# Performance work log

Hardware: AMD Instinct MI355X
Metric: run time of the kernel (lower is better)

## Reference

```python
import jax, jax.numpy as jnp
import numpy as np

S, B, I, H, L = 512, 64, 512, 512, 2
EPS = 1e-5


def setup_inputs() -> dict:
    key = jax.random.key(0)
    ks = jax.random.split(key, 8)
    gain = float(np.sqrt(1.0 / H))
    u = lambda k, shp: jax.random.uniform(k, shp, jnp.float32, -gain, gain)
    return {
        "inputs": jax.random.normal(ks[0], (S, B, I), jnp.float32),
        "h0": jnp.zeros((L, B, H), jnp.float32),
        "c0": jnp.zeros((L, B, H), jnp.float32),
        "wx0": u(ks[1], (I, 4 * H)),
        "wx1": u(ks[2], (H, 4 * H)),
        "wh0": u(ks[3], (H, 4 * H)),
        "wh1": u(ks[4], (H, 4 * H)),
        "bias": u(ks[5], (L, 4 * H)),
        "ln_gamma": jnp.ones((L, 4, H), jnp.float32),
        "ln_beta": jnp.zeros((L, 4, H), jnp.float32),
    }


def _layer(x, h, c, wx, wh, b, gamma, beta):
    # Precompute the input projection as one big GEMM: [S,B,4H]
    xg = jnp.einsum('sbi,ig->sbg', x, wx) + b

    def cell(carry, xg_t):
        h, c = carry
        gate = xg_t + h @ wh                      # [B, 4H]
        g = gate.reshape(B, 4, H)
        mu = jnp.mean(g, axis=-1, keepdims=True)
        var = jnp.var(g, axis=-1, keepdims=True)
        g = (g - mu) * jax.lax.rsqrt(var + EPS) * gamma + beta
        i, f, o, u = g[:, 0], g[:, 1], g[:, 2], g[:, 3]
        c = jax.nn.sigmoid(f) * c + jax.nn.sigmoid(i) * jnp.tanh(u)
        h = jax.nn.sigmoid(o) * jnp.tanh(c)
        return (h, c), h

    (h, c), ys = jax.lax.scan(cell, (h, c), xg)
    return ys, h, c


def reference(inputs, h0, c0, wx0, wx1, wh0, wh1, bias, ln_gamma, ln_beta):
    x = inputs
    wxs, whs = [wx0, wx1], [wh0, wh1]
    hs, cs = [], []
    for l in range(L):
        x, h, c = _layer(x, h0[l], c0[l], wxs[l], whs[l], bias[l], ln_gamma[l], ln_beta[l])
        hs.append(h)
        cs.append(c)
    return x, jnp.stack(hs, 0), jnp.stack(cs, 0)
```

## Files before the change

### kernel.cpp

```cpp
#include <hip/hip_runtime.h>


#define NTH 256

typedef float f32x4 __attribute__((ext_vector_type(4)));

__device__ __forceinline__ float sigm(float x) { return 1.f / (1.f + __expf(-x)); }
__device__ __forceinline__ float tanh_f(float x) { return 2.f / (1.f + __expf(-2.f * x)) - 1.f; }

__device__ __forceinline__ unsigned long long pack2(float a, float b) {
  union { float f[2]; unsigned long long u; } x; x.f[0] = a; x.f[1] = b; return x.u;
}
__device__ __forceinline__ float lo2(unsigned long long u) {
  union { unsigned long long u; float f[2]; } x; x.u = u; return x.f[0];
}
__device__ __forceinline__ float hi2(unsigned long long u) {
  union { unsigned long long u; float f[2]; } x; x.u = u; return x.f[1];
}
__device__ __forceinline__ void sys_store64(unsigned long long* p, unsigned long long v) {
  __hip_atomic_store(p, v, __ATOMIC_RELAXED, __HIP_MEMORY_SCOPE_SYSTEM);
}
__device__ __forceinline__ unsigned long long sys_load64(const unsigned long long* p) {
  return __hip_atomic_load(p, __ATOMIC_RELAXED, __HIP_MEMORY_SCOPE_SYSTEM);
}

__device__ __forceinline__ void post(unsigned int* flag, unsigned int val) {
  __syncthreads();
  if (threadIdx.x == 0)
    __hip_atomic_store(flag, val, __ATOMIC_RELEASE, __HIP_MEMORY_SCOPE_SYSTEM);
}

__device__ __forceinline__ void waitall(const unsigned int* flags, unsigned int target) {
  long guard = 0;
  for (;;) {
    int ok = 1;
    if (threadIdx.x < 128) {
      unsigned int v = __hip_atomic_load(&flags[threadIdx.x * 32],
                                         __ATOMIC_RELAXED, __HIP_MEMORY_SCOPE_SYSTEM);
      ok = (v >= target);
    }
    if (__syncthreads_and(ok)) break;
    if (++guard > (1L << 22)) break;
  }
  __atomic_signal_fence(__ATOMIC_ACQUIRE);
}

__global__ __launch_bounds__(NTH, 1)
void lstm_pk(const float* __restrict__ inputs, const float* __restrict__ h0,
             const float* __restrict__ c0,
             const float* __restrict__ wx0, const float* __restrict__ wx1,
             const float* __restrict__ wh0, const float* __restrict__ wh1,
             const float* __restrict__ bias, const float* __restrict__ gamma_,
             const float* __restrict__ beta_,
             float* __restrict__ out,
             unsigned int* flags,
             unsigned long long* slots,
             float* __restrict__ h_state)
{
  extern __shared__ float lds[];
  float* W_lds = lds;
  float* A_lds = lds + 16384;
  float* part  = lds + 16384 + 17408;
  float* gates = part + 4352;
  float* minv  = gates + 1024;

  const int tid = threadIdx.x;
  const int wg = blockIdx.x;
  const int layer = wg >> 7;
  const int w = wg & 127;
  const int wavet = tid >> 6;
  const int lane = tid & 63;
  const int rq = lane & 15;
  const int gq = lane >> 4;
  const int srow = tid >> 2;
  const int sg = tid & 3;
  const int hc = 4 * w + sg;

  const float* Wx = layer ? wx1 : wx0;
  const float* Wh = layer ? wh1 : wh0;

  for (int i = 0; i < 16; ++i) {
    int e = tid + i * 256;
    int k = e >> 2, g = e & 3;
    const float* src = (k < 512) ? (Wx + (size_t)k * 2048)
                                 : (Wh + (size_t)(k - 512) * 2048);
    f32x4 v = *(const f32x4*)(src + g * 512 + 4 * w);
    *(f32x4*)&W_lds[k * 16 + g * 4] = v;
  }

  f32x4 biasr = *(const f32x4*)(bias + layer * 2048 + sg * 512 + 4 * w);
  float gam[4], bet[4];
#pragma unroll
  for (int g = 0; g < 4; ++g) {
    gam[g] = gamma_[layer * 2048 + g * 512 + hc];
    bet[g] = beta_[layer * 2048 + g * 512 + hc];
  }
  float c_st = c0[layer * 32768 + srow * 512 + hc];

  unsigned long long* slotL = slots + (size_t)layer * 32768;
  float* hstL = h_state + layer * 32768;
  unsigned int* fmyL = flags + layer * 4096;
  unsigned int* myflag = fmyL + w * 32;
  const unsigned int* fL0 = flags;

  const int strow = rq + 16 * wavet;
  const int first = layer ? 4 : 0;

  for (int t = 0; t < 512; ++t) {
    const unsigned int t2 = 2u * (unsigned)t;
    const float* xsrc = (layer ? out : inputs) + (size_t)t * 32768;
    const float* hsrc = (t == 0) ? (h0 + layer * 32768) : hstL;

    if (layer == 1 && t > 0) waitall(fmyL, t2);

    f32x4 acc[4];
#pragma unroll
    for (int r = 0; r < 4; ++r) acc[r] = (f32x4){0.f, 0.f, 0.f, 0.f};

    f32x4 st[8];
    auto LOADC = [&](int c) {
      const int koff = (c & 3) * 128;
      if (c < 4 && layer == 0) {
        const float* src = xsrc + strow * 512 + koff;
#pragma unroll
        for (int i = 0; i < 8; ++i) {
          int kq = gq + 4 * i;
          st[i] = *(const f32x4*)(src + 4 * kq);
        }
      } else {
        const float* src = ((c >= 4) ? hsrc : xsrc) + strow * 512 + koff;
        const unsigned long long* s64 = (const unsigned long long*)src;
#pragma unroll
        for (int i = 0; i < 8; ++i) {
          int kq = gq + 4 * i;
          unsigned long long a = sys_load64(&s64[2 * kq]);
          unsigned long long b = sys_load64(&s64[2 * kq + 1]);
          st[i][0] = lo2(a); st[i][1] = hi2(a);
          st[i][2] = lo2(b); st[i][3] = hi2(b);
        }
      }
    };
    auto WRITEC = [&](int b) {
      float* dst = A_lds + b * 8704;
#pragma unroll
      for (int i = 0; i < 8; ++i) {
        int kq = gq + 4 * i;
#pragma unroll
        for (int j = 0; j < 4; ++j)
          dst[(4 * kq + j) * 68 + strow] = st[i][j];
      }
    };
    auto COMPUTEC = [&](int c, int b) {
      const float* Ab = A_lds + b * 8704;
      const int kg = c * 128 + wavet * 32;
#pragma unroll 8
      for (int kk = 0; kk < 32; ++kk) {
        int k = wavet * 32 + kk;
        f32x4 av = *(const f32x4*)&Ab[k * 68 + 4 * rq];
        f32x4 wv = *(const f32x4*)&W_lds[(kg + kk) * 16 + gq * 4];
        acc[0] += av[0] * wv;
        acc[1] += av[1] * wv;
        acc[2] += av[2] * wv;
        acc[3] += av[3] * wv;
      }
    };

    LOADC(first);
    WRITEC(0);
    __syncthreads();
#pragma unroll 1
    for (int co = 0; co < 8; ++co) {
      int c = (co + first) & 7;
      if (co < 7) {
        if (co == 3) {
          if (layer == 1) waitall(fL0, t2 + 2u);
          else if (t > 0) waitall(fmyL, t2);
        }
        LOADC((c + 1) & 7);
      }
      COMPUTEC(c, co & 1);
      if (co < 7) WRITEC((co + 1) & 1);
      __syncthreads();
    }

#pragma unroll
    for (int r = 0; r < 4; ++r)
#pragma unroll
      for (int cc = 0; cc < 4; ++cc)
        part[(wavet * 64 + 4 * rq + r) * 17 + gq * 4 + cc] = acc[r][cc];
    __syncthreads();

    {
      f32x4 pre;
#pragma unroll
      for (int cc = 0; cc < 4; ++cc) {
        float v = biasr[cc];
        v += part[(0 * 64 + srow) * 17 + sg * 4 + cc];
        v += part[(1 * 64 + srow) * 17 + sg * 4 + cc];
        v += part[(2 * 64 + srow) * 17 + sg * 4 + cc];
        v += part[(3 * 64 + srow) * 17 + sg * 4 + cc];
        pre[cc] = v;
      }
      *(f32x4*)&gates[srow * 16 + sg * 4] = pre;
      float s = ((pre[0] + pre[1]) + pre[2]) + pre[3];
      float ss = ((pre[0] * pre[0] + pre[1] * pre[1]) + pre[2] * pre[2]) + pre[3] * pre[3];
      sys_store64(&slotL[(size_t)w * 256 + tid], pack2(s, ss));
    }
    post(myflag, t2 + 1u);
    waitall(fmyL, t2 + 1u);

    {
      float Sc[8], SSc[8];
#pragma unroll
      for (int j = 0; j < 8; ++j) { Sc[j] = 0.f; SSc[j] = 0.f; }
#pragma unroll 4
      for (int q8 = 0; q8 < 16; ++q8) {
#pragma unroll
        for (int j = 0; j < 8; ++j) {
          unsigned long long u = sys_load64(&slotL[(size_t)(q8 * 8 + j) * 256 + tid]);
          Sc[j] += lo2(u); SSc[j] += hi2(u);
        }
      }
      float S = ((Sc[0] + Sc[1]) + (Sc[2] + Sc[3])) + ((Sc[4] + Sc[5]) + (Sc[6] + Sc[7]));
      float SS = ((SSc[0] + SSc[1]) + (SSc[2] + SSc[3])) + ((SSc[4] + SSc[5]) + (SSc[6] + SSc[7]));
      float mu = S * (1.f / 512.f);
      float var = SS * (1.f / 512.f) - mu * mu;
      minv[tid * 2 + 0] = mu;
      minv[tid * 2 + 1] = rsqrtf(fmaxf(var, 0.f) + 1e-5f);
    }
    __syncthreads();

    {
      float gv[4];
#pragma unroll
      for (int g = 0; g < 4; ++g) {
        float pre = gates[srow * 16 + g * 4 + sg];
        gv[g] = (pre - minv[(srow * 4 + g) * 2]) * minv[(srow * 4 + g) * 2 + 1] * gam[g] + bet[g];
      }
      float ig = sigm(gv[0]);
      float fg = sigm(gv[1]);
      float og = sigm(gv[2]);
      float ug = tanh_f(gv[3]);
      c_st = fg * c_st + ig * ug;
      float hv = og * tanh_f(c_st);

      float hv2 = __shfl_down(hv, 1);
      float cv2 = __shfl_down(c_st, 1);
      if ((sg & 1) == 0) {
        unsigned long long hp = pack2(hv, hv2);
        sys_store64((unsigned long long*)&hstL[srow * 512 + hc], hp);
        sys_store64((unsigned long long*)&out[(size_t)t * 32768 + srow * 512 + hc], hp);
        if (t == 511) {
          sys_store64((unsigned long long*)&out[16777216 + layer * 32768 + srow * 512 + hc], hp);
          sys_store64((unsigned long long*)&out[16842752 + layer * 32768 + srow * 512 + hc],
                      pack2(c_st, cv2));
        }
      }
    }
    post(myflag, t2 + 2u);
  }
}

extern "C" void kernel_launch(void* const* d_in, const int* in_sizes, int n_in,
                              void* d_out, int out_size, void* d_ws, size_t ws_size,
                              hipStream_t stream) {
  const float* inputs = (const float*)d_in[0];
  const float* h0 = (const float*)d_in[1];
  const float* c0 = (const float*)d_in[2];
  const float* wx0 = (const float*)d_in[3];
  const float* wx1 = (const float*)d_in[4];
  const float* wh0 = (const float*)d_in[5];
  const float* wh1 = (const float*)d_in[6];
  const float* bias = (const float*)d_in[7];
  const float* gamma_ = (const float*)d_in[8];
  const float* beta_ = (const float*)d_in[9];
  float* out = (float*)d_out;

  char* ws = (char*)d_ws;
  unsigned int* flags = (unsigned int*)ws;
  unsigned long long* slots = (unsigned long long*)(ws + 65536);
  float* h_state = (float*)(ws + 65536 + 524288);

  const int smem_bytes = 158720;
  hipFuncSetAttribute((const void*)lstm_pk,
                      hipFuncAttributeMaxDynamicSharedMemorySize, smem_bytes);
  hipMemsetAsync(ws, 0, 65536, stream);

  hipLaunchKernelGGL(lstm_pk, dim3(256), dim3(NTH), smem_bytes, stream,
                     inputs, h0, c0, wx0, wx1, wh0, wh1, bias, gamma_, beta_,
                     out, flags, slots, h_state);
}
```

Measured before the change: 21.61 ms.

## Use fixed-point atomic LN stat reduction and retile per-step GEMM with smaller chunks

The layer-norm statistics are now reduced with 64-bit fixed-point atomicAdds into a double-buffered global accumulator. Previously each of 128 workgroups wrote its partial sums to slots and every workgroup then read all 128 of them. The per-timestep GEMM is retiled: 64-wide K chunks (16 per step), an 8x8 register tile per thread, a split-K partial reduction through LDS, and plain vector loads instead of system-scope atomic loads, with acquire fences added after the waits. This is meant to cut the cross-workgroup reduction traffic and the latency per timestep. In exchange it adds quantization error in the statistics and atomic contention on shared addresses. It also relies on zeroing the next step's buffer while other workgroups may still be using it.

```diff
diff --git a/kernel.cpp b/kernel.cpp
--- a/kernel.cpp
+++ b/kernel.cpp
@@ -8,20 +8,14 @@
 __device__ __forceinline__ float sigm(float x) { return 1.f / (1.f + __expf(-x)); }
 __device__ __forceinline__ float tanh_f(float x) { return 2.f / (1.f + __expf(-2.f * x)) - 1.f; }
 
+__device__ __forceinline__ void sys_store64(unsigned long long* p, unsigned long long v) {
+  __hip_atomic_store(p, v, __ATOMIC_RELAXED, __HIP_MEMORY_SCOPE_SYSTEM);
+}
+__device__ __forceinline__ unsigned long long sys_load64(const unsigned long long* p) {
+  return __hip_atomic_load(p, __ATOMIC_RELAXED, __HIP_MEMORY_SCOPE_SYSTEM);
+}
 __device__ __forceinline__ unsigned long long pack2(float a, float b) {
   union { float f[2]; unsigned long long u; } x; x.f[0] = a; x.f[1] = b; return x.u;
-}
-__device__ __forceinline__ float lo2(unsigned long long u) {
-  union { unsigned long long u; float f[2]; } x; x.u = u; return x.f[0];
-}
-__device__ __forceinline__ float hi2(unsigned long long u) {
-  union { unsigned long long u; float f[2]; } x; x.u = u; return x.f[1];
-}
-__device__ __forceinline__ void sys_store64(unsigned long long* p, unsigned long long v) {
-  __hip_atomic_store(p, v, __ATOMIC_RELAXED, __HIP_MEMORY_SCOPE_SYSTEM);
-}
-__device__ __forceinline__ unsigned long long sys_load64(const unsigned long long* p) {
-  return __hip_atomic_load(p, __ATOMIC_RELAXED, __HIP_MEMORY_SCOPE_SYSTEM);
 }
 
 __device__ __forceinline__ void post(unsigned int* flag, unsigned int val) {
@@ -54,24 +48,25 @@
              const float* __restrict__ beta_,
              float* __restrict__ out,
              unsigned int* flags,
-             unsigned long long* slots,
+             unsigned long long* stat_ws,
              float* __restrict__ h_state)
 {
   extern __shared__ float lds[];
   float* W_lds = lds;
   float* A_lds = lds + 16384;
-  float* part  = lds + 16384 + 17408;
-  float* gates = part + 4352;
+  float* part  = lds + 16384 + 8704;
+  float* gates = part + 8704;
   float* minv  = gates + 1024;
 
   const int tid = threadIdx.x;
   const int wg = blockIdx.x;
   const int layer = wg >> 7;
   const int w = wg & 127;
-  const int wavet = tid >> 6;
-  const int lane = tid & 63;
-  const int rq = lane & 15;
-  const int gq = lane >> 4;
+  const int cb = tid & 1;
+  const int ra = (tid >> 1) & 7;
+  const int m  = tid >> 4;
+  const int strow = tid & 63;
+  const int kq4 = tid >> 6;
   const int srow = tid >> 2;
   const int sg = tid & 3;
   const int hc = 4 * w + sg;
@@ -97,71 +92,68 @@
   }
   float c_st = c0[layer * 32768 + srow * 512 + hc];
 
-  unsigned long long* slotL = slots + (size_t)layer * 32768;
   float* hstL = h_state + layer * 32768;
   unsigned int* fmyL = flags + layer * 4096;
   unsigned int* myflag = fmyL + w * 32;
   const unsigned int* fL0 = flags;
 
-  const int strow = rq + 16 * wavet;
-  const int first = layer ? 4 : 0;
+  const int first = layer ? 8 : 0;
 
   for (int t = 0; t < 512; ++t) {
     const unsigned int t2 = 2u * (unsigned)t;
     const float* xsrc = (layer ? out : inputs) + (size_t)t * 32768;
     const float* hsrc = (t == 0) ? (h0 + layer * 32768) : hstL;
-
-    if (layer == 1 && t > 0) waitall(fmyL, t2);
-
-    f32x4 acc[4];
-#pragma unroll
-    for (int r = 0; r < 4; ++r) acc[r] = (f32x4){0.f, 0.f, 0.f, 0.f};
-
-    f32x4 st[8];
+    unsigned long long* statbuf = stat_ws + ((size_t)(t & 1) * 2 + layer) * 512;
+
+    if (layer == 1) {
+      waitall(fmyL, t2);
+      __builtin_amdgcn_fence(__ATOMIC_ACQUIRE, "agent");
+    }
+
+    f32x4 acc[8][2];
+#pragma unroll
+    for (int r = 0; r < 8; ++r) {
+      acc[r][0] = (f32x4){0.f, 0.f, 0.f, 0.f};
+      acc[r][1] = (f32x4){0.f, 0.f, 0.f, 0.f};
+    }
+
+    f32x4 st[4];
     auto LOADC = [&](int c) {
-      const int koff = (c & 3) * 128;
-      if (c < 4 && layer == 0) {
-        const float* src = xsrc + strow * 512 + koff;
-#pragma unroll
-        for (int i = 0; i < 8; ++i) {
-          int kq = gq + 4 * i;
-          st[i] = *(const f32x4*)(src + 4 * kq);
-        }
-      } else {
-        const float* src = ((c >= 4) ? hsrc : xsrc) + strow * 512 + koff;
-        const unsigned long long* s64 = (const unsigned long long*)src;
-#pragma unroll
-        for (int i = 0; i < 8; ++i) {
-          int kq = gq + 4 * i;
-          unsigned long long a = sys_load64(&s64[2 * kq]);
-          unsigned long long b = sys_load64(&s64[2 * kq + 1]);
-          st[i][0] = lo2(a); st[i][1] = hi2(a);
-          st[i][2] = lo2(b); st[i][3] = hi2(b);
-        }
-      }
+      const float* src = (c >= 8) ? (hsrc + strow * 512 + (c - 8) * 64)
+                                  : (xsrc + strow * 512 + c * 64);
+#pragma unroll
+      for (int i = 0; i < 4; ++i)
+        st[i] = *(const f32x4*)(src + 4 * (kq4 + 4 * i));
     };
     auto WRITEC = [&](int b) {
-      float* dst = A_lds + b * 8704;
-#pragma unroll
-      for (int i = 0; i < 8; ++i) {
-        int kq = gq + 4 * i;
+      float* dst = A_lds + b * 4352;
+#pragma unroll
+      for (int i = 0; i < 4; ++i) {
+        int kk = 4 * (kq4 + 4 * i);
 #pragma unroll
         for (int j = 0; j < 4; ++j)
-          dst[(4 * kq + j) * 68 + strow] = st[i][j];
+          dst[(kk + j) * 68 + strow] = st[i][j];
       }
     };
     auto COMPUTEC = [&](int c, int b) {
-      const float* Ab = A_lds + b * 8704;
-      const int kg = c * 128 + wavet * 32;
-#pragma unroll 8
-      for (int kk = 0; kk < 32; ++kk) {
-        int k = wavet * 32 + kk;
-        f32x4 av = *(const f32x4*)&Ab[k * 68 + 4 * rq];
-        f32x4 wv = *(const f32x4*)&W_lds[(kg + kk) * 16 + gq * 4];
-        acc[0] += av[0] * wv;
-        acc[1] += av[1] * wv;
-        acc[2] += av[2] * wv;
-        acc[3] += av[3] * wv;
+      const float* Ab = A_lds + b * 4352;
+      const int kW = (c < 8 ? c * 64 : 512 + (c - 8) * 64) + 4 * m;
+      const int kA = 4 * m;
+#pragma unroll
+      for (int kk = 0; kk < 4; ++kk) {
+        const float* arow = &Ab[(kA + kk) * 68 + 8 * ra];
+        f32x4 av0 = *(const f32x4*)arow;
+        f32x4 av1 = *(const f32x4*)(arow + 4);
+        const float* wrow = &W_lds[(kW + kk) * 16 + 8 * cb];
+        f32x4 wv0 = *(const f32x4*)wrow;
+        f32x4 wv1 = *(const f32x4*)(wrow + 4);
+#pragma unroll
+        for (int r = 0; r < 4; ++r) {
+          acc[r][0] += av0[r] * wv0;
+          acc[r][1] += av0[r] * wv1;
+          acc[r + 4][0] += av1[r] * wv0;
+          acc[r + 4][1] += av1[r] * wv1;
+        }
       }
     };
 
@@ -169,64 +161,77 @@
     WRITEC(0);
     __syncthreads();
 #pragma unroll 1
-    for (int co = 0; co < 8; ++co) {
-      int c = (co + first) & 7;
-      if (co < 7) {
-        if (co == 3) {
-          if (layer == 1) waitall(fL0, t2 + 2u);
-          else if (t > 0) waitall(fmyL, t2);
+    for (int co = 0; co < 16; ++co) {
+      int c = (co + first) & 15;
+      if (co < 15) {
+        if (co == 7) {
+          if (layer == 1) {
+            waitall(fL0, t2 + 2u);
+            __builtin_amdgcn_fence(__ATOMIC_ACQUIRE, "agent");
+          } else {
+            waitall(fmyL, t2);
+            __builtin_amdgcn_fence(__ATOMIC_ACQUIRE, "agent");
+          }
         }
-        LOADC((c + 1) & 7);
+        LOADC((c + 1) & 15);
       }
       COMPUTEC(c, co & 1);
-      if (co < 7) WRITEC((co + 1) & 1);
+      if (co < 15) WRITEC((co + 1) & 1);
       __syncthreads();
     }
 
-#pragma unroll
-    for (int r = 0; r < 4; ++r)
-#pragma unroll
-      for (int cc = 0; cc < 4; ++cc)
-        part[(wavet * 64 + 4 * rq + r) * 17 + gq * 4 + cc] = acc[r][cc];
-    __syncthreads();
-
-    {
-      f32x4 pre;
-#pragma unroll
-      for (int cc = 0; cc < 4; ++cc) {
-        float v = biasr[cc];
-        v += part[(0 * 64 + srow) * 17 + sg * 4 + cc];
-        v += part[(1 * 64 + srow) * 17 + sg * 4 + cc];
-        v += part[(2 * 64 + srow) * 17 + sg * 4 + cc];
-        v += part[(3 * 64 + srow) * 17 + sg * 4 + cc];
-        pre[cc] = v;
-      }
+    if (m >= 8) {
+      float* pg = part + (size_t)(m - 8) * 1088;
+#pragma unroll
+      for (int r = 0; r < 8; ++r) {
+        *(f32x4*)&pg[(8 * ra + r) * 17 + 8 * cb] = acc[r][0];
+        *(f32x4*)&pg[(8 * ra + r) * 17 + 8 * cb + 4] = acc[r][1];
+      }
+    }
+    __syncthreads();
+    if (m < 8) {
+      float* pg = part + (size_t)m * 1088;
+#pragma unroll
+      for (int r = 0; r < 8; ++r) {
+        float* p0 = &pg[(8 * ra + r) * 17 + 8 * cb];
+        f32x4 v0 = *(f32x4*)p0 + acc[r][0];
+        f32x4 v1 = *(f32x4*)(p0 + 4) + acc[r][1];
+        *(f32x4*)p0 = v0;
+        *(f32x4*)(p0 + 4) = v1;
+      }
+    }
+    __syncthreads();
+
+    {
+      f32x4 pre = biasr;
+#pragma unroll
+      for (int g = 0; g < 8; ++g)
+        pre += *(const f32x4*)&part[(size_t)g * 1088 + srow * 17 + sg * 4];
       *(f32x4*)&gates[srow * 16 + sg * 4] = pre;
       float s = ((pre[0] + pre[1]) + pre[2]) + pre[3];
       float ss = ((pre[0] * pre[0] + pre[1] * pre[1]) + pre[2] * pre[2]) + pre[3] * pre[3];
-      sys_store64(&slotL[(size_t)w * 256 + tid], pack2(s, ss));
+      atomicAdd(&statbuf[2 * tid],
+                (unsigned long long)(long long)llrintf(s * 1048576.f));
+      atomicAdd(&statbuf[2 * tid + 1],
+                (unsigned long long)(long long)llrintf(ss * 1048576.f));
     }
     post(myflag, t2 + 1u);
     waitall(fmyL, t2 + 1u);
 
     {
-      float Sc[8], SSc[8];
-#pragma unroll
-      for (int j = 0; j < 8; ++j) { Sc[j] = 0.f; SSc[j] = 0.f; }
-#pragma unroll 4
-      for (int q8 = 0; q8 < 16; ++q8) {
-#pragma unroll
-        for (int j = 0; j < 8; ++j) {
-          unsigned long long u = sys_load64(&slotL[(size_t)(q8 * 8 + j) * 256 + tid]);
-          Sc[j] += lo2(u); SSc[j] += hi2(u);
-        }
-      }
-      float S = ((Sc[0] + Sc[1]) + (Sc[2] + Sc[3])) + ((Sc[4] + Sc[5]) + (Sc[6] + Sc[7]));
-      float SS = ((SSc[0] + SSc[1]) + (SSc[2] + SSc[3])) + ((SSc[4] + SSc[5]) + (SSc[6] + SSc[7]));
-      float mu = S * (1.f / 512.f);
-      float var = SS * (1.f / 512.f) - mu * mu;
-      minv[tid * 2 + 0] = mu;
-      minv[tid * 2 + 1] = rsqrtf(fmaxf(var, 0.f) + 1e-5f);
+      unsigned long long* zb = stat_ws + ((size_t)((t + 1) & 1) * 2 + layer) * 512;
+      if (tid < 4) sys_store64(&zb[4 * w + tid], 0ull);
+    }
+
+    {
+      long long S = (long long)sys_load64(&statbuf[2 * tid]);
+      long long SS = (long long)sys_load64(&statbuf[2 * tid + 1]);
+      float Sf = (float)S * (1.f / 1048576.f);
+      float SSf = (float)SS * (1.f / 1048576.f);
+      float mu = Sf * (1.f / 512.f);
+      float var = SSf * (1.f / 512.f) - mu * mu;
+      minv[2 * tid + 0] = mu;
+      minv[2 * tid + 1] = rsqrtf(fmaxf(var, 0.f) + 1e-5f);
     }
     __syncthreads();
 
@@ -278,15 +283,15 @@
 
   char* ws = (char*)d_ws;
   unsigned int* flags = (unsigned int*)ws;
-  unsigned long long* slots = (unsigned long long*)(ws + 65536);
-  float* h_state = (float*)(ws + 65536 + 524288);
-
-  const int smem_bytes = 158720;
+  unsigned long long* stat_ws = (unsigned long long*)(ws + 65536);
+  float* h_state = (float*)(ws + 65536 + 16384);
+
+  const int smem_bytes = 141312;
   hipFuncSetAttribute((const void*)lstm_pk,
                       hipFuncAttributeMaxDynamicSharedMemorySize, smem_bytes);
-  hipMemsetAsync(ws, 0, 65536, stream);
+  hipMemsetAsync(ws, 0, 65536 + 16384, stream);
 
   hipLaunchKernelGGL(lstm_pk, dim3(256), dim3(NTH), smem_bytes, stream,
                      inputs, h0, c0, wx0, wx1, wh0, wh1, bias, gamma_, beta_,
-                     out, flags, slots, h_state);
-}
+                     out, flags, stat_ws, h_state);
+}
```

After: 21.67 ms. Within noise of the previous version (+0.3%).

## Overlap next-step input projection with LayerNorm stat exchange; use plain loads after fences

Applied to the files above, without the earlier changes.

Splits each step's gate GEMM into an input part (x·Wx) and a recurrent part (h·Wh). The x·Wx part for step t+1 is computed while waiting for the cross-block LayerNorm statistics barrier of step t, which takes it off the serial recurrent path. System-scope atomic 64-bit loads are replaced by ordinary vector loads preceded by agent-scope acquire fences. This relies on the fences being enough for cross-block visibility, and it keeps an extra accumulator set live in registers.

```diff
diff --git a/kernel.cpp b/kernel.cpp
--- a/kernel.cpp
+++ b/kernel.cpp
@@ -11,17 +11,8 @@
 __device__ __forceinline__ unsigned long long pack2(float a, float b) {
   union { float f[2]; unsigned long long u; } x; x.f[0] = a; x.f[1] = b; return x.u;
 }
-__device__ __forceinline__ float lo2(unsigned long long u) {
-  union { unsigned long long u; float f[2]; } x; x.u = u; return x.f[0];
-}
-__device__ __forceinline__ float hi2(unsigned long long u) {
-  union { unsigned long long u; float f[2]; } x; x.u = u; return x.f[1];
-}
 __device__ __forceinline__ void sys_store64(unsigned long long* p, unsigned long long v) {
   __hip_atomic_store(p, v, __ATOMIC_RELAXED, __HIP_MEMORY_SCOPE_SYSTEM);
-}
-__device__ __forceinline__ unsigned long long sys_load64(const unsigned long long* p) {
-  return __hip_atomic_load(p, __ATOMIC_RELAXED, __HIP_MEMORY_SCOPE_SYSTEM);
 }
 
 __device__ __forceinline__ void post(unsigned int* flag, unsigned int val) {
@@ -104,90 +95,80 @@
   const unsigned int* fL0 = flags;
 
   const int strow = rq + 16 * wavet;
-  const int first = layer ? 4 : 0;
-
-  for (int t = 0; t < 512; ++t) {
-    const unsigned int t2 = 2u * (unsigned)t;
-    const float* xsrc = (layer ? out : inputs) + (size_t)t * 32768;
-    const float* hsrc = (t == 0) ? (h0 + layer * 32768) : hstL;
-
-    if (layer == 1 && t > 0) waitall(fmyL, t2);
-
-    f32x4 acc[4];
-#pragma unroll
-    for (int r = 0; r < 4; ++r) acc[r] = (f32x4){0.f, 0.f, 0.f, 0.f};
-
-    f32x4 st[8];
-    auto LOADC = [&](int c) {
-      const int koff = (c & 3) * 128;
-      if (c < 4 && layer == 0) {
-        const float* src = xsrc + strow * 512 + koff;
-#pragma unroll
-        for (int i = 0; i < 8; ++i) {
-          int kq = gq + 4 * i;
-          st[i] = *(const f32x4*)(src + 4 * kq);
-        }
-      } else {
-        const float* src = ((c >= 4) ? hsrc : xsrc) + strow * 512 + koff;
-        const unsigned long long* s64 = (const unsigned long long*)src;
-#pragma unroll
-        for (int i = 0; i < 8; ++i) {
-          int kq = gq + 4 * i;
-          unsigned long long a = sys_load64(&s64[2 * kq]);
-          unsigned long long b = sys_load64(&s64[2 * kq + 1]);
-          st[i][0] = lo2(a); st[i][1] = hi2(a);
-          st[i][2] = lo2(b); st[i][3] = hi2(b);
-        }
-      }
-    };
-    auto WRITEC = [&](int b) {
-      float* dst = A_lds + b * 8704;
-#pragma unroll
-      for (int i = 0; i < 8; ++i) {
-        int kq = gq + 4 * i;
-#pragma unroll
-        for (int j = 0; j < 4; ++j)
-          dst[(4 * kq + j) * 68 + strow] = st[i][j];
-      }
-    };
-    auto COMPUTEC = [&](int c, int b) {
-      const float* Ab = A_lds + b * 8704;
-      const int kg = c * 128 + wavet * 32;
+
+  f32x4 st[8];
+  auto LOADC = [&](const float* src, int koff) {
+    const float* s = src + strow * 512 + koff;
+#pragma unroll
+    for (int i = 0; i < 8; ++i)
+      st[i] = *(const f32x4*)(s + 4 * (gq + 4 * i));
+  };
+  auto WRITEC = [&](int b) {
+    float* dst = A_lds + b * 8704;
+#pragma unroll
+    for (int i = 0; i < 8; ++i) {
+      int kq = gq + 4 * i;
+#pragma unroll
+      for (int j = 0; j < 4; ++j)
+        dst[(4 * kq + j) * 68 + strow] = st[i][j];
+    }
+  };
+  auto COMPUTEC = [&](int kW, int b, f32x4* acc) {
+    const float* Ab = A_lds + b * 8704;
+    const int kg = kW + wavet * 32;
 #pragma unroll 8
-      for (int kk = 0; kk < 32; ++kk) {
-        int k = wavet * 32 + kk;
-        f32x4 av = *(const f32x4*)&Ab[k * 68 + 4 * rq];
-        f32x4 wv = *(const f32x4*)&W_lds[(kg + kk) * 16 + gq * 4];
-        acc[0] += av[0] * wv;
-        acc[1] += av[1] * wv;
-        acc[2] += av[2] * wv;
-        acc[3] += av[3] * wv;
-      }
-    };
-
-    LOADC(first);
+    for (int kk = 0; kk < 32; ++kk) {
+      int k = wavet * 32 + kk;
+      f32x4 av = *(const f32x4*)&Ab[k * 68 + 4 * rq];
+      f32x4 wv = *(const f32x4*)&W_lds[(kg + kk) * 16 + gq * 4];
+      acc[0] += av[0] * wv;
+      acc[1] += av[1] * wv;
+      acc[2] += av[2] * wv;
+      acc[3] += av[3] * wv;
+    }
+  };
+  auto GEMM4 = [&](const float* src, int wbase, f32x4* acc) {
+    LOADC(src, 0);
     WRITEC(0);
     __syncthreads();
 #pragma unroll 1
-    for (int co = 0; co < 8; ++co) {
-      int c = (co + first) & 7;
-      if (co < 7) {
-        if (co == 3) {
-          if (layer == 1) waitall(fL0, t2 + 2u);
-          else if (t > 0) waitall(fmyL, t2);
-        }
-        LOADC((c + 1) & 7);
-      }
-      COMPUTEC(c, co & 1);
-      if (co < 7) WRITEC((co + 1) & 1);
+    for (int i = 0; i < 4; ++i) {
+      if (i < 3) LOADC(src, (i + 1) * 128);
+      COMPUTEC(wbase + i * 128, i & 1, acc);
+      if (i < 3) WRITEC((i + 1) & 1);
       __syncthreads();
     }
+  };
+
+  f32x4 acc_x[4];
+#pragma unroll
+  for (int r = 0; r < 4; ++r) acc_x[r] = (f32x4){0.f, 0.f, 0.f, 0.f};
+  if (layer == 0) {
+    GEMM4(inputs, 0, acc_x);
+  } else {
+    waitall(fL0, 2u);
+    __builtin_amdgcn_fence(__ATOMIC_ACQUIRE, "agent");
+    GEMM4(out, 0, acc_x);
+  }
+
+  for (int t = 0; t < 512; ++t) {
+    const unsigned int t2 = 2u * (unsigned)t;
+    const float* hsrc = (t == 0) ? (h0 + layer * 32768) : hstL;
+
+    if (t) {
+      waitall(fmyL, t2);
+      __builtin_amdgcn_fence(__ATOMIC_ACQUIRE, "agent");
+    }
+    f32x4 acc_h[4];
+#pragma unroll
+    for (int r = 0; r < 4; ++r) acc_h[r] = (f32x4){0.f, 0.f, 0.f, 0.f};
+    GEMM4(hsrc, 512, acc_h);
 
 #pragma unroll
     for (int r = 0; r < 4; ++r)
 #pragma unroll
       for (int cc = 0; cc < 4; ++cc)
-        part[(wavet * 64 + 4 * rq + r) * 17 + gq * 4 + cc] = acc[r][cc];
+        part[(wavet * 64 + 4 * rq + r) * 17 + gq * 4 + cc] = acc_h[r][cc] + acc_x[r][cc];
     __syncthreads();
 
     {
@@ -207,7 +188,20 @@
       sys_store64(&slotL[(size_t)w * 256 + tid], pack2(s, ss));
     }
     post(myflag, t2 + 1u);
+
+#pragma unroll
+    for (int r = 0; r < 4; ++r) acc_x[r] = (f32x4){0.f, 0.f, 0.f, 0.f};
+    if (t < 511) {
+      if (layer == 1) {
+        waitall(fL0, t2 + 4u);
+        __builtin_amdgcn_fence(__ATOMIC_ACQUIRE, "agent");
+      }
+      const float* xn = (layer ? out : inputs) + (size_t)(t + 1) * 32768;
+      GEMM4(xn, 0, acc_x);
+    }
+
     waitall(fmyL, t2 + 1u);
+    __builtin_amdgcn_fence(__ATOMIC_ACQUIRE, "agent");
 
     {
       float Sc[8], SSc[8];
@@ -217,8 +211,10 @@
       for (int q8 = 0; q8 < 16; ++q8) {
 #pragma unroll
         for (int j = 0; j < 8; ++j) {
-          unsigned long long u = sys_load64(&slotL[(size_t)(q8 * 8 + j) * 256 + tid]);
-          Sc[j] += lo2(u); SSc[j] += hi2(u);
+          unsigned long long u = *(const unsigned long long*)
+              &slotL[(size_t)(q8 * 8 + j) * 256 + tid];
+          union { unsigned long long u; float f[2]; } x; x.u = u;
+          Sc[j] += x.f[0]; SSc[j] += x.f[1];
         }
       }
       float S = ((Sc[0] + Sc[1]) + (Sc[2] + Sc[3])) + ((Sc[4] + Sc[5]) + (Sc[6] + Sc[7]));
```

Measured after the change: 22.01 ms. About the same (+1.8%).
